# Kernel optimization log

Measured on AMD Instinct MI355X. Metric: run time of the kernel, lower is better.

The kernel has to match this reference:

```python
import math
import jax, jax.numpy as jnp
import numpy as np

MAX_N = 16  # matches init kwarg max_n

def _mn_lists():
    m_list, n_list = [], []
    for i in range(MAX_N):
        for j in range(i + 1):
            m_list.append(j)
            n_list.append(i)
    return np.array(m_list), np.array(n_list)

M_ARR, N_ARR = _mn_lists()  # option='all': all (m, n) pairs with 0 <= m <= n < MAX_N
# scipy sph_harm normalization: sqrt((2n+1)/(4pi) * (n-m)!/(n+m)!)
COEFF = np.array([
    math.sqrt((2 * n + 1) / (4 * math.pi) * math.factorial(n - m) / math.factorial(n + m))
    for m, n in zip(M_ARR, N_ARR)
], dtype=np.float32)
M_ZERO = (M_ARR == 0)


def setup_inputs() -> dict:
    key = jax.random.key(0)
    xyz = jax.random.normal(key, (500000, 3), dtype=jnp.float32)
    return {"xyz": xyz}


def _sph_harm_real(xyz):
    # Normalize direction vectors
    r = jnp.linalg.norm(xyz, axis=-1, keepdims=True)
    u = xyz / r
    ct = u[:, 2]                       # cos(phi), phi = polar angle
    st = jnp.sqrt(jnp.clip(1.0 - ct * ct, 0.0))  # sin(phi) >= 0 since phi in [0, pi]
    theta = jnp.arctan2(-u[:, 1], -u[:, 0]) + math.pi  # azimuth, as in original module

    # Associated Legendre P_n^m(cos phi) with Condon-Shortley phase (scipy lpmv convention)
    # via standard stable recurrences; loops are over the small fixed (n, m) grid.
    P = {}
    for m in range(MAX_N):
        if m == 0:
            P[(0, 0)] = jnp.ones_like(ct)
        else:
            # P_m^m = -(2m-1) * sin(phi) * P_{m-1}^{m-1}  (includes (-1)^m phase)
            P[(m, m)] = -(2 * m - 1) * st * P[(m - 1, m - 1)]
        if m + 1 < MAX_N:
            P[(m + 1, m)] = (2 * m + 1) * ct * P[(m, m)]
        for n in range(m + 2, MAX_N):
            P[(n, m)] = ((2 * n - 1) * ct * P[(n - 1, m)] - (n + m - 1) * P[(n - 2, m)]) / (n - m)

    Pstack = jnp.stack([P[(n, m)] for m, n in zip(M_ARR, N_ARR)], axis=1)  # [N, pairs]
    mtheta = theta[:, None] * jnp.asarray(M_ARR, dtype=theta.dtype)[None, :]  # [N, pairs]
    coeff = jnp.asarray(COEFF)
    harm_re = coeff * Pstack * jnp.cos(mtheta)
    harm_im = coeff * Pstack * jnp.sin(mtheta)

    mz = jnp.asarray(M_ZERO)
    out = jnp.concatenate([harm_re[:, M_ZERO], harm_re[:, ~M_ZERO], harm_im[:, ~M_ZERO]], axis=1)
    return out.astype(jnp.float32)


def reference(xyz):
    return _sph_harm_real(xyz)
```

## Files before the change

kernel.cpp:

```cpp
#include <hip/hip_runtime.h>


#define NMAX   16
#define BLOCK  64
#define HALF   128
#define PAD    129

constexpr double cfact(int k) { double r = 1.0; for (int i = 2; i <= k; ++i) r *= (double)i; return r; }
constexpr double csqrt_(double x) {
    double g = x > 1.0 ? x : 1.0;
    for (int i = 0; i < 120; ++i) g = 0.5 * (g + x / g);
    return g;
}
constexpr double PI_ = 3.14159265358979323846;

struct CoefTab { float c[NMAX][NMAX]; };
constexpr CoefTab make_coef() {
    CoefTab t{};
    for (int n = 0; n < NMAX; ++n)
        for (int m = 0; m <= n; ++m)
            t.c[n][m] = (float)csqrt_(((2.0 * n + 1.0) / (4.0 * PI_)) * cfact(n - m) / cfact(n + m));
    return t;
}
constexpr CoefTab COEF = make_coef();

template <int PASS>
__device__ __forceinline__ void stage(float* rowPtr, int col, float v) {
    constexpr int lo = PASS * HALF;
    if (col >= lo && col < lo + HALF) {
        int c = col - lo;
        rowPtr[(c >> 2) + ((c & 3) << 5)] = v;
    }
}

template <int PASS>
__device__ __forceinline__ void emit(float* rowPtr, int n, int m, float p, float cm, float sm) {
    float v = COEF.c[n][m] * p;
    if (m == 0) {
        stage<PASS>(rowPtr, n, v);
    } else {
        int col = 16 + (n * (n - 1)) / 2 + (m - 1);
        stage<PASS>(rowPtr, col, v * cm);
        stage<PASS>(rowPtr, col + 120, v * sm);
    }
}

template <int PASS>
__device__ __forceinline__ void compute_stage(float ct, float st, float c1, float s1, float* rowPtr) {
    float pmm = 1.0f;
    float cm = 1.0f, sm = 0.0f;
#pragma unroll
    for (int m = 0; m < NMAX; ++m) {
        emit<PASS>(rowPtr, m, m, pmm, cm, sm);
        float pn2 = pmm;
        if (m < NMAX - 1) {
            float pn1 = (float)(2 * m + 1) * ct * pmm;
            emit<PASS>(rowPtr, m + 1, m, pn1, cm, sm);
#pragma unroll
            for (int n = m + 2; n < NMAX; ++n) {
                float pn = ((float)(2 * n - 1) * ct * pn1 - (float)(n + m - 1) * pn2)
                           * (1.0f / (float)(n - m));
                emit<PASS>(rowPtr, n, m, pn, cm, sm);
                pn2 = pn1;
                pn1 = pn;
            }
        }
        pmm = -(float)(2 * m + 1) * st * pmm;
        float cn = cm * c1 - sm * s1;
        sm = sm * c1 + cm * s1;
        cm = cn;
    }
}

template <int PASS>
__device__ __forceinline__ void flush(const float* tile, float* out, long long rowBase, int npts, int t) {
#pragma unroll
    for (int k = 0; k < 32; ++k) {
        int flat4 = k * 64 + t;
        int row   = flat4 >> 5;
        int c4    = flat4 & 31;
        long long grow = rowBase + row;
        if (grow < (long long)npts) {
            const float* p = tile + row * PAD + c4;
            float4 v = make_float4(p[0], p[32], p[64], p[96]);
            *reinterpret_cast<float4*>(out + grow * 256 + PASS * HALF + 4 * c4) = v;
        }
    }
}

__global__ __launch_bounds__(BLOCK)
void sph_harm_kernel(const float* __restrict__ xyz, float* __restrict__ out, int npts) {
    __shared__ float tile[BLOCK * PAD];
    const int t = threadIdx.x;
    const long long rowBase = (long long)blockIdx.x * BLOCK;
    long long pt = rowBase + t;
    long long cpt = pt < npts ? pt : (long long)npts - 1;

    float x = xyz[3 * cpt + 0];
    float y = xyz[3 * cpt + 1];
    float z = xyz[3 * cpt + 2];

    float r2 = x * x + y * y + z * z;
    float r  = sqrtf(r2);
    float ct = z / r;
    float st = sqrtf(fmaxf(1.0f - ct * ct, 0.0f));

    float rho2 = x * x + y * y;
    float c1, s1;
    if (rho2 > 0.0f) {
        float rinv = 1.0f / sqrtf(rho2);
        c1 = x * rinv;
        s1 = y * rinv;
    } else {
        c1 = 1.0f;
        s1 = 0.0f;
    }

    float* rowPtr = tile + t * PAD;

    compute_stage<0>(ct, st, c1, s1, rowPtr);
    __syncthreads();
    flush<0>(tile, out, rowBase, npts, t);
    __syncthreads();
    compute_stage<1>(ct, st, c1, s1, rowPtr);
    __syncthreads();
    flush<1>(tile, out, rowBase, npts, t);
}

extern "C" void kernel_launch(void* const* d_in, const int* in_sizes, int n_in,
                              void* d_out, int out_size, void* d_ws, size_t ws_size,
                              hipStream_t stream) {
    const float* xyz = (const float*)d_in[0];
    float* out = (float*)d_out;
    int npts = in_sizes[0] / 3;
    int blocks = (npts + BLOCK - 1) / BLOCK;
    hipLaunchKernelGGL(sph_harm_kernel, dim3(blocks), dim3(BLOCK), 0, stream,
                       xyz, out, npts);
}
```

Measured before the change: 511.2 us.

## Split LDS staging into four quarter passes and drop block barriers for wave fences

Output rows are now staged through shared memory in four 64-column passes instead of two 128-column passes. The tile shrinks to 64x65 floats and flush reads contiguous float4 values per row. Because the block is a single 64-thread wavefront, __syncthreads is replaced by an s_waitcnt lgkmcnt(0) fence, and bounds checks are skipped for non-tail blocks. The smaller LDS footprint should raise occupancy and cut barrier overhead. The cost is recomputing the Legendre recurrence four times instead of twice, and correctness now relies on the block being exactly one wave.

```diff
diff --git a/kernel.cpp b/kernel.cpp
--- a/kernel.cpp
+++ b/kernel.cpp
@@ -3,8 +3,8 @@
 
 #define NMAX   16
 #define BLOCK  64
-#define HALF   128
-#define PAD    129
+#define QCOLS  64
+#define STRIDE 65
 
 constexpr double cfact(int k) { double r = 1.0; for (int i = 2; i <= k; ++i) r *= (double)i; return r; }
 constexpr double csqrt_(double x) {
@@ -24,12 +24,15 @@
 }
 constexpr CoefTab COEF = make_coef();
 
+__device__ __forceinline__ void wave_lds_fence() {
+    asm volatile("s_waitcnt lgkmcnt(0)" ::: "memory");
+}
+
 template <int PASS>
 __device__ __forceinline__ void stage(float* rowPtr, int col, float v) {
-    constexpr int lo = PASS * HALF;
-    if (col >= lo && col < lo + HALF) {
-        int c = col - lo;
-        rowPtr[(c >> 2) + ((c & 3) << 5)] = v;
+    constexpr int lo = PASS * QCOLS;
+    if (col >= lo && col < lo + QCOLS) {
+        rowPtr[col - lo] = v;
     }
 }
 
@@ -73,28 +76,30 @@
 }
 
 template <int PASS>
-__device__ __forceinline__ void flush(const float* tile, float* out, long long rowBase, int npts, int t) {
+__device__ __forceinline__ void flush(const float* tile, float* out,
+                                      long long rowBase, int npts, int t, bool tail) {
+    const int hi = t >> 4;
+    const int c4 = t & 15;
+    const float* p0 = tile + hi * STRIDE + 4 * c4;
+    float* o0 = out + (rowBase + hi) * 256 + PASS * QCOLS + 4 * c4;
 #pragma unroll
-    for (int k = 0; k < 32; ++k) {
-        int flat4 = k * 64 + t;
-        int row   = flat4 >> 5;
-        int c4    = flat4 & 31;
-        long long grow = rowBase + row;
-        if (grow < (long long)npts) {
-            const float* p = tile + row * PAD + c4;
-            float4 v = make_float4(p[0], p[32], p[64], p[96]);
-            *reinterpret_cast<float4*>(out + grow * 256 + PASS * HALF + 4 * c4) = v;
+    for (int it = 0; it < 16; ++it) {
+        if (!tail || (rowBase + it * 4 + hi) < (long long)npts) {
+            const float* p = p0 + it * (4 * STRIDE);
+            float4 v = make_float4(p[0], p[1], p[2], p[3]);
+            *reinterpret_cast<float4*>(o0 + it * 4 * 256) = v;
         }
     }
 }
 
 __global__ __launch_bounds__(BLOCK)
 void sph_harm_kernel(const float* __restrict__ xyz, float* __restrict__ out, int npts) {
-    __shared__ float tile[BLOCK * PAD];
+    __shared__ float tile[BLOCK * STRIDE];
     const int t = threadIdx.x;
     const long long rowBase = (long long)blockIdx.x * BLOCK;
     long long pt = rowBase + t;
     long long cpt = pt < npts ? pt : (long long)npts - 1;
+    const bool tail = (rowBase + BLOCK) > (long long)npts;
 
     float x = xyz[3 * cpt + 0];
     float y = xyz[3 * cpt + 1];
@@ -116,15 +121,26 @@
         s1 = 0.0f;
     }
 
-    float* rowPtr = tile + t * PAD;
+    float* rowPtr = tile + t * STRIDE;
 
     compute_stage<0>(ct, st, c1, s1, rowPtr);
-    __syncthreads();
-    flush<0>(tile, out, rowBase, npts, t);
-    __syncthreads();
+    wave_lds_fence();
+    flush<0>(tile, out, rowBase, npts, t, tail);
+    wave_lds_fence();
+
     compute_stage<1>(ct, st, c1, s1, rowPtr);
-    __syncthreads();
-    flush<1>(tile, out, rowBase, npts, t);
+    wave_lds_fence();
+    flush<1>(tile, out, rowBase, npts, t, tail);
+    wave_lds_fence();
+
+    compute_stage<2>(ct, st, c1, s1, rowPtr);
+    wave_lds_fence();
+    flush<2>(tile, out, rowBase, npts, t, tail);
+    wave_lds_fence();
+
+    compute_stage<3>(ct, st, c1, s1, rowPtr);
+    wave_lds_fence();
+    flush<3>(tile, out, rowBase, npts, t, tail);
 }
 
 extern "C" void kernel_launch(void* const* d_in, const int* in_sizes, int n_in,
```

Result: no change. 510.0 us (-0.2%).

## Split each point across four lanes, each staging one 64-column quarter

Applied to the files above, without the earlier changes.

Each block now handles 16 points with four threads per point. Every thread still computes the full Legendre/trig recurrence, but writes only its own 64-column quarter of the output row to LDS. Writes to the other quarters go to a per-thread dump slot. The two-pass compute/flush scheme with block barriers is replaced by a single pass followed by an LDS waitcnt fence, since the block is one wave. The intent is more parallelism and fewer barriers, at the cost of four-fold redundant arithmetic per point and a non-coalesced float4 LDS read pattern with stride 257.

```diff
diff --git a/kernel.cpp b/kernel.cpp
--- a/kernel.cpp
+++ b/kernel.cpp
@@ -3,8 +3,10 @@
 
 #define NMAX   16
 #define BLOCK  64
-#define HALF   128
-#define PAD    129
+#define PPB    16
+#define STRIDE 257
+#define DUMPO  (PPB * STRIDE)
+#define TILEF  (DUMPO + 128)
 
 constexpr double cfact(int k) { double r = 1.0; for (int i = 2; i <= k; ++i) r *= (double)i; return r; }
 constexpr double csqrt_(double x) {
@@ -24,43 +26,46 @@
 }
 constexpr CoefTab COEF = make_coef();
 
-template <int PASS>
-__device__ __forceinline__ void stage(float* rowPtr, int col, float v) {
-    constexpr int lo = PASS * HALF;
-    if (col >= lo && col < lo + HALF) {
-        int c = col - lo;
-        rowPtr[(c >> 2) + ((c & 3) << 5)] = v;
+__device__ __forceinline__ void wave_lds_fence() {
+    asm volatile("s_waitcnt lgkmcnt(0)" ::: "memory");
+}
+
+__device__ __forceinline__ void stageq(float* b0, float* b1, float* b2, float* b3,
+                                       int col, float v) {
+    const int q   = col >> 6;
+    const int off = col & 63;
+    float* b = (q == 0) ? b0 : (q == 1) ? b1 : (q == 2) ? b2 : b3;
+    b[off] = v;
+}
+
+__device__ __forceinline__ void emit(float* b0, float* b1, float* b2, float* b3,
+                                     int n, int m, float p, float cm, float sm) {
+    float v = COEF.c[n][m] * p;
+    if (m == 0) {
+        stageq(b0, b1, b2, b3, n, v);
+    } else {
+        int col = 16 + (n * (n - 1)) / 2 + (m - 1);
+        stageq(b0, b1, b2, b3, col,       v * cm);
+        stageq(b0, b1, b2, b3, col + 120, v * sm);
     }
 }
 
-template <int PASS>
-__device__ __forceinline__ void emit(float* rowPtr, int n, int m, float p, float cm, float sm) {
-    float v = COEF.c[n][m] * p;
-    if (m == 0) {
-        stage<PASS>(rowPtr, n, v);
-    } else {
-        int col = 16 + (n * (n - 1)) / 2 + (m - 1);
-        stage<PASS>(rowPtr, col, v * cm);
-        stage<PASS>(rowPtr, col + 120, v * sm);
-    }
-}
-
-template <int PASS>
-__device__ __forceinline__ void compute_stage(float ct, float st, float c1, float s1, float* rowPtr) {
+__device__ __forceinline__ void compute_stage(float ct, float st, float c1, float s1,
+                                              float* b0, float* b1, float* b2, float* b3) {
     float pmm = 1.0f;
     float cm = 1.0f, sm = 0.0f;
 #pragma unroll
     for (int m = 0; m < NMAX; ++m) {
-        emit<PASS>(rowPtr, m, m, pmm, cm, sm);
+        emit(b0, b1, b2, b3, m, m, pmm, cm, sm);
         float pn2 = pmm;
         if (m < NMAX - 1) {
             float pn1 = (float)(2 * m + 1) * ct * pmm;
-            emit<PASS>(rowPtr, m + 1, m, pn1, cm, sm);
+            emit(b0, b1, b2, b3, m + 1, m, pn1, cm, sm);
 #pragma unroll
             for (int n = m + 2; n < NMAX; ++n) {
                 float pn = ((float)(2 * n - 1) * ct * pn1 - (float)(n + m - 1) * pn2)
                            * (1.0f / (float)(n - m));
-                emit<PASS>(rowPtr, n, m, pn, cm, sm);
+                emit(b0, b1, b2, b3, n, m, pn, cm, sm);
                 pn2 = pn1;
                 pn1 = pn;
             }
@@ -72,28 +77,14 @@
     }
 }
 
-template <int PASS>
-__device__ __forceinline__ void flush(const float* tile, float* out, long long rowBase, int npts, int t) {
-#pragma unroll
-    for (int k = 0; k < 32; ++k) {
-        int flat4 = k * 64 + t;
-        int row   = flat4 >> 5;
-        int c4    = flat4 & 31;
-        long long grow = rowBase + row;
-        if (grow < (long long)npts) {
-            const float* p = tile + row * PAD + c4;
-            float4 v = make_float4(p[0], p[32], p[64], p[96]);
-            *reinterpret_cast<float4*>(out + grow * 256 + PASS * HALF + 4 * c4) = v;
-        }
-    }
-}
-
 __global__ __launch_bounds__(BLOCK)
 void sph_harm_kernel(const float* __restrict__ xyz, float* __restrict__ out, int npts) {
-    __shared__ float tile[BLOCK * PAD];
-    const int t = threadIdx.x;
-    const long long rowBase = (long long)blockIdx.x * BLOCK;
-    long long pt = rowBase + t;
+    __shared__ float tile[TILEF];
+    const int t   = threadIdx.x;
+    const int p   = t >> 2;
+    const int sub = t & 3;
+    const long long row0 = (long long)blockIdx.x * PPB;
+    long long pt  = row0 + p;
     long long cpt = pt < npts ? pt : (long long)npts - 1;
 
     float x = xyz[3 * cpt + 0];
@@ -116,15 +107,27 @@
         s1 = 0.0f;
     }
 
-    float* rowPtr = tile + t * PAD;
+    float* rowQ = tile + p * STRIDE + sub * 64;
+    float* dump = tile + DUMPO + t;
+    float* b0 = (sub == 0) ? rowQ : dump;
+    float* b1 = (sub == 1) ? rowQ : dump;
+    float* b2 = (sub == 2) ? rowQ : dump;
+    float* b3 = (sub == 3) ? rowQ : dump;
 
-    compute_stage<0>(ct, st, c1, s1, rowPtr);
-    __syncthreads();
-    flush<0>(tile, out, rowBase, npts, t);
-    __syncthreads();
-    compute_stage<1>(ct, st, c1, s1, rowPtr);
-    __syncthreads();
-    flush<1>(tile, out, rowBase, npts, t);
+    compute_stage(ct, st, c1, s1, b0, b1, b2, b3);
+
+    wave_lds_fence();
+
+    const bool tail = (row0 + PPB) > (long long)npts;
+    float* o0 = out + row0 * 256 + 4 * t;
+#pragma unroll
+    for (int it = 0; it < PPB; ++it) {
+        if (!tail || (row0 + it) < (long long)npts) {
+            const float* q = tile + it * STRIDE + 4 * t;
+            float4 v = make_float4(q[0], q[1], q[2], q[3]);
+            *reinterpret_cast<float4*>(o0 + it * 256) = v;
+        }
+    }
 }
 
 extern "C" void kernel_launch(void* const* d_in, const int* in_sizes, int n_in,
@@ -133,7 +136,7 @@
     const float* xyz = (const float*)d_in[0];
     float* out = (float*)d_out;
     int npts = in_sizes[0] / 3;
-    int blocks = (npts + BLOCK - 1) / BLOCK;
+    int blocks = (npts + PPB - 1) / PPB;
     hipLaunchKernelGGL(sph_harm_kernel, dim3(blocks), dim3(BLOCK), 0, stream,
                        xyz, out, npts);
 }
```

Measured after the change: 506.6 us. Within noise of the previous version (-0.9%).
